# Kernel optimization log

Measured on AMD Instinct MI355X. Metric: run time of the kernel, lower is better.

## Reference

```python
import jax, jax.numpy as jnp
import numpy as np

N_NODES = 500000
N_EDGES = 16000000
IN_DIM = 17


def setup_inputs() -> dict:
    key = jax.random.key(0)
    k1, k2, k3, k4, k5, k6, k7 = jax.random.split(key, 7)
    x = jax.random.normal(k1, (N_NODES, IN_DIM), dtype=jnp.float32)
    edge_index = jax.random.randint(k2, (2, N_EDGES), 0, N_NODES, dtype=jnp.int64)
    edge_weight = jax.random.uniform(k3, (N_EDGES,), dtype=jnp.float32)
    # SAGEConv(17, 1): lin_l applied to aggregated neighbors (with bias),
    # lin_r applied to root features (no bias, PyG convention).
    s = 1.0 / np.sqrt(IN_DIM)
    w_l = jax.random.uniform(k4, (1, IN_DIM), minval=-s, maxval=s, dtype=jnp.float32)
    b_l = jax.random.uniform(k5, (1,), minval=-s, maxval=s, dtype=jnp.float32)
    w_r = jax.random.uniform(k6, (1, IN_DIM), minval=-s, maxval=s, dtype=jnp.float32)
    # out: Linear(1, 1)
    k8, k9 = jax.random.split(k7)
    w_o = jax.random.uniform(k8, (1, 1), minval=-1.0, maxval=1.0, dtype=jnp.float32)
    b_o = jax.random.uniform(k9, (1,), minval=-1.0, maxval=1.0, dtype=jnp.float32)
    return {"x": x, "edge_index": edge_index, "edge_weight": edge_weight,
            "w_l": w_l, "b_l": b_l, "w_r": w_r, "w_o": w_o, "b_o": b_o}


def reference(x, edge_index, edge_weight, w_l, b_l, w_r, w_o, b_o):
    # SAGEConv (mean aggregation). edge_weight is unused (faithful to PyG SAGEConv).
    # Project to out_dim=1 BEFORE aggregation (linearity makes this exact and
    # avoids materializing a [E,17] gathered buffer):
    #   lin_l(mean_j x_j) + b_l == mean_j (x_j @ W_l^T) + b_l
    src, dst = edge_index[0], edge_index[1]
    x_proj_l = x @ w_l.T                      # [N, 1]
    msg = x_proj_l[src, 0]                    # [E]  gathered source projections
    agg = jax.ops.segment_sum(msg, dst, num_segments=x.shape[0])          # [N]
    cnt = jax.ops.segment_sum(jnp.ones_like(msg), dst, num_segments=x.shape[0])
    mean = agg / jnp.maximum(cnt, 1.0)        # zero for isolated nodes
    h = mean[:, None] + b_l + x @ w_r.T       # [N, 1]  lin_l(aggr) + lin_r(x)
    h = jax.nn.elu(h)
    return h @ w_o.T + b_o                    # [N, 1]
```

## Files before the change

kernel.cpp:

```cpp
#include <hip/hip_runtime.h>
#include <hip/hip_bf16.h>
#include <math.h>

#define IN_DIM 17
#define NB 128
#define LOG_BN 12
#define BN 4096
#define K_SPLIT 16
#define CHUNK 8192
#define EPT 32
#define VAL_SCALE 4096.0f
#define FP_SCALE 268435456.0f
#define FP_INV   (1.0 / 268435456.0)

__global__ void node_proj_kernel(const float* __restrict__ x,
                                 const float* __restrict__ w_l,
                                 const float* __restrict__ w_r,
                                 float* __restrict__ p_l,
                                 float* __restrict__ p_r,
                                 int n_nodes) {
    int i = blockIdx.x * blockDim.x + threadIdx.x;
    if (i >= n_nodes) return;
    const float* row = x + (size_t)i * IN_DIM;
    float sl = 0.0f, sr = 0.0f;
#pragma unroll
    for (int k = 0; k < IN_DIM; ++k) {
        float v = row[k];
        sl = fmaf(v, w_l[k], sl);
        sr = fmaf(v, w_r[k], sr);
    }
    p_l[i] = sl;
    p_r[i] = sr;
}

__global__ __launch_bounds__(256, 4)
void sort_scatter_kernel(const int* __restrict__ src,
                         const int* __restrict__ dst,
                         const float* __restrict__ p_l,
                         unsigned* __restrict__ staging,
                         unsigned short* __restrict__ segtab,
                         int n_edges) {
    __shared__ unsigned cnt[NB];
    __shared__ unsigned sstart[NB + 1];
    __shared__ unsigned lbuf[CHUNK];

    const int tid = threadIdx.x;
    const int blk = blockIdx.x;
    const int e0 = blk * CHUNK;
    const int chunk_n = min(CHUNK, n_edges - e0);
    const int nvec = chunk_n >> 2;

    for (int t = tid; t < NB; t += 256) cnt[t] = 0;
    __syncthreads();

    uint4 dreg[EPT / 4];
    uint4 sreg[EPT / 4];
    unsigned rpack[EPT / 2];
    const uint4* dv = (const uint4*)(dst + e0);
    const uint4* sv = (const uint4*)(src + e0);
#pragma unroll
    for (int k = 0; k < EPT / 4; ++k) {
        int q = tid + k * 256;
        if (q < nvec) {
            uint4 d = dv[q];
            dreg[k] = d;
            sreg[k] = sv[q];
            unsigned r0 = atomicAdd(&cnt[d.x >> LOG_BN], 1u);
            unsigned r1 = atomicAdd(&cnt[d.y >> LOG_BN], 1u);
            unsigned r2 = atomicAdd(&cnt[d.z >> LOG_BN], 1u);
            unsigned r3 = atomicAdd(&cnt[d.w >> LOG_BN], 1u);
            rpack[2 * k]     = r0 | (r1 << 16);
            rpack[2 * k + 1] = r2 | (r3 << 16);
        }
    }
    unsigned tail_rank = 0;
    {
        int i = (nvec << 2) + tid;
        if (i < chunk_n)
            tail_rank = atomicAdd(&cnt[(unsigned)dst[e0 + i] >> LOG_BN], 1u);
    }
    __syncthreads();

    if (tid < 64) {
        unsigned c0 = cnt[tid], c1 = cnt[tid + 64];
        unsigned s0 = c0;
#pragma unroll
        for (int off = 1; off < 64; off <<= 1) {
            unsigned v = __shfl_up(s0, off);
            if (tid >= off) s0 += v;
        }
        unsigned tot0 = __shfl(s0, 63);
        unsigned s1 = c1;
#pragma unroll
        for (int off = 1; off < 64; off <<= 1) {
            unsigned v = __shfl_up(s1, off);
            if (tid >= off) s1 += v;
        }
        s1 += tot0;
        sstart[tid + 1] = s0;
        sstart[tid + 65] = s1;
        if (tid == 0) sstart[0] = 0;
    }
    __syncthreads();

    for (int t = tid; t <= NB; t += 256)
        segtab[(size_t)blk * (NB + 2) + t] = (unsigned short)sstart[t];

#pragma unroll
    for (int k = 0; k < EPT / 4; ++k) {
        int q = tid + k * 256;
        if (q < nvec) {
            uint4 s = sreg[k];
            uint4 d = dreg[k];
            float pf[4] = {p_l[s.x], p_l[s.y], p_l[s.z], p_l[s.w]};
            unsigned dd[4] = {d.x, d.y, d.z, d.w};
            unsigned rk[4] = {rpack[2 * k] & 0xFFFFu, rpack[2 * k] >> 16,
                              rpack[2 * k + 1] & 0xFFFFu, rpack[2 * k + 1] >> 16};
#pragma unroll
            for (int u = 0; u < 4; ++u) {
                int fx = __float2int_rn(pf[u] * VAL_SCALE);
                fx = max(-32768, min(32767, fx));
                unsigned entry = ((unsigned)(fx & 0xFFFF) << 16) | (dd[u] & (BN - 1));
                unsigned b = dd[u] >> LOG_BN;
                lbuf[sstart[b] + rk[u]] = entry;
            }
        }
    }
    {
        int i = (nvec << 2) + tid;
        if (i < chunk_n) {
            unsigned s = (unsigned)src[e0 + i];
            unsigned d = (unsigned)dst[e0 + i];
            int fx = __float2int_rn(p_l[s] * VAL_SCALE);
            fx = max(-32768, min(32767, fx));
            unsigned entry = ((unsigned)(fx & 0xFFFF) << 16) | (d & (BN - 1));
            lbuf[sstart[d >> LOG_BN] + tail_rank] = entry;
        }
    }
    __syncthreads();

    uint4* outp = (uint4*)(staging + (size_t)blk * CHUNK);
    const uint4* lp = (const uint4*)lbuf;
    int nv4 = (chunk_n + 3) >> 2;
    for (int q = tid; q < nv4; q += 256)
        outp[q] = lp[q];
}

__global__ __launch_bounds__(256, 4)
void reduce_kernel(const unsigned* __restrict__ staging,
                   const unsigned short* __restrict__ segtab,
                   unsigned* __restrict__ bins,
                   int nblk) {
    __shared__ unsigned lds_p[BN];
    const int tid = threadIdx.x;
    const int b = blockIdx.x / K_SPLIT;
    const int j = blockIdx.x % K_SPLIT;
    const int wave = tid >> 6, lane = tid & 63;

    for (int i = tid; i < BN; i += 256) lds_p[i] = 0u;
    __syncthreads();

    const int blk0 = (int)((long long)nblk * j / K_SPLIT);
    const int blk1 = (int)((long long)nblk * (j + 1) / K_SPLIT);

    int blk = blk0 + wave;
    unsigned sA = 0, eA = 0, sB = 0, eB = 0;
    unsigned enA0 = 0, enA1 = 0;
    if (blk < blk1) {
        const unsigned short* st = segtab + (size_t)blk * (NB + 2) + b;
        sA = st[0]; eA = st[1];
    }
    if (blk + 4 < blk1) {
        const unsigned short* st = segtab + (size_t)(blk + 4) * (NB + 2) + b;
        sB = st[0]; eB = st[1];
    }
    if (blk < blk1) {
        const unsigned* sp = staging + (size_t)blk * CHUNK;
        unsigned i0 = sA + lane;
        if (i0 < eA) enA0 = sp[i0];
        unsigned i1 = i0 + 64;
        if (i1 < eA) enA1 = sp[i1];
    }

    while (blk < blk1) {
        unsigned sC = 0, eC = 0;
        if (blk + 8 < blk1) {
            const unsigned short* st = segtab + (size_t)(blk + 8) * (NB + 2) + b;
            sC = st[0]; eC = st[1];
        }
        unsigned enB0 = 0, enB1 = 0;
        if (blk + 4 < blk1) {
            const unsigned* spn = staging + (size_t)(blk + 4) * CHUNK;
            unsigned i0 = sB + lane;
            if (i0 < eB) enB0 = spn[i0];
            unsigned i1 = i0 + 64;
            if (i1 < eB) enB1 = spn[i1];
        }
        {
            unsigned i0 = sA + lane;
            if (i0 < eA) {
                int v = (int)(short)(enA0 >> 16);
                atomicAdd(&lds_p[enA0 & (BN - 1)], ((unsigned)v << 8) | 1u);
            }
            unsigned i1 = i0 + 64;
            if (i1 < eA) {
                int v = (int)(short)(enA1 >> 16);
                atomicAdd(&lds_p[enA1 & (BN - 1)], ((unsigned)v << 8) | 1u);
            }
            if (sA + 128 < eA) {
                const unsigned* sp = staging + (size_t)blk * CHUNK;
                for (unsigned i = sA + 128 + lane; i < eA; i += 64) {
                    unsigned en = sp[i];
                    int v = (int)(short)(en >> 16);
                    atomicAdd(&lds_p[en & (BN - 1)], ((unsigned)v << 8) | 1u);
                }
            }
        }
        asm volatile("" :: "v"(enB0), "v"(enB1), "v"(sC), "v"(eC));
        blk += 4;
        sA = sB; eA = eB; enA0 = enB0; enA1 = enB1;
        sB = sC; eB = eC;
    }
    __syncthreads();
    unsigned* gb = bins + (size_t)b * BN;
    for (int i = tid; i < BN; i += 256) {
        unsigned v = lds_p[i];
        if (v) atomicAdd(&gb[i], v);
    }
}

__global__ void finalize_kernel(const float* __restrict__ p_r,
                                const unsigned* __restrict__ bins,
                                const float* __restrict__ b_l,
                                const float* __restrict__ w_o,
                                const float* __restrict__ b_o,
                                float* __restrict__ out,
                                int n_nodes) {
    int i = blockIdx.x * blockDim.x + threadIdx.x;
    if (i >= n_nodes) return;
    unsigned u = bins[i];
    int sum24 = ((int)u) >> 8;
    int cnt = (int)(u & 0xFFu);
    float sum = (float)sum24 * (1.0f / VAL_SCALE);
    float mean = sum / fmaxf((float)cnt, 1.0f);
    float h = mean + b_l[0] + p_r[i];
    h = (h > 0.0f) ? h : expm1f(h);
    out[i] = fmaf(h, w_o[0], b_o[0]);
}

__global__ void edge_scatter_fb(const int* __restrict__ edge_index,
                                const float* __restrict__ p_l,
                                unsigned long long* __restrict__ bins,
                                int n_edges) {
    int e = blockIdx.x * blockDim.x + threadIdx.x;
    if (e >= n_edges) return;
    int s = edge_index[e];
    int d = edge_index[n_edges + e];
    float p = p_l[s];
    long long sfx = (long long)llrintf(p * FP_SCALE);
    unsigned long long delta = ((unsigned long long)sfx << 20) | 1ULL;
    atomicAdd(&bins[d], delta);
}

__global__ void finalize_fb(const float* __restrict__ p_r,
                            const unsigned long long* __restrict__ bins,
                            const float* __restrict__ b_l,
                            const float* __restrict__ w_o,
                            const float* __restrict__ b_o,
                            float* __restrict__ out,
                            int n_nodes) {
    int i = blockIdx.x * blockDim.x + threadIdx.x;
    if (i >= n_nodes) return;
    long long packed = (long long)bins[i];
    int cntv = (int)(packed & 0xFFFFFLL);
    long long sfx = packed >> 20;
    float sum = (float)((double)sfx * FP_INV);
    float mean = sum / fmaxf((float)cntv, 1.0f);
    float h = mean + b_l[0] + p_r[i];
    h = (h > 0.0f) ? h : expm1f(h);
    out[i] = fmaf(h, w_o[0], b_o[0]);
}

static inline size_t align_up(size_t v, size_t a) { return (v + a - 1) & ~(a - 1); }

extern "C" void kernel_launch(void* const* d_in, const int* in_sizes, int n_in,
                              void* d_out, int out_size, void* d_ws, size_t ws_size,
                              hipStream_t stream) {
    const float* x   = (const float*)d_in[0];
    const int*   ei  = (const int*)d_in[1];
    const float* w_l = (const float*)d_in[3];
    const float* b_l = (const float*)d_in[4];
    const float* w_r = (const float*)d_in[5];
    const float* w_o = (const float*)d_in[6];
    const float* b_o = (const float*)d_in[7];
    float* out = (float*)d_out;

    const int n_nodes = in_sizes[0] / IN_DIM;
    const int n_edges = in_sizes[2];
    const int* src = ei;
    const int* dst = ei + n_edges;
    const int nblk = (n_edges + CHUNK - 1) / CHUNK;

    char* ws = (char*)d_ws;
    size_t off = 0;
    size_t o_pl = off;      off = align_up(off + (size_t)n_nodes * 4, 256);
    size_t o_pr = off;      off = align_up(off + (size_t)n_nodes * 4, 256);
    size_t o_stage = off;   off = align_up(off + (size_t)nblk * CHUNK * 4, 256);
    size_t o_seg = off;     off = align_up(off + (size_t)nblk * (NB + 2) * 2, 256);
    size_t o_bins = off;    off = align_up(off + (size_t)NB * BN * 4, 256);
    size_t need = off;

    float* p_l = (float*)(ws + o_pl);
    float* p_r = (float*)(ws + o_pr);

    const int B = 256;
    node_proj_kernel<<<(n_nodes + B - 1) / B, B, 0, stream>>>(x, w_l, w_r, p_l, p_r, n_nodes);

    if (ws_size >= need) {
        unsigned* staging       = (unsigned*)(ws + o_stage);
        unsigned short* segtab  = (unsigned short*)(ws + o_seg);
        unsigned* bins          = (unsigned*)(ws + o_bins);

        hipMemsetAsync(bins, 0, (size_t)NB * BN * 4, stream);
        sort_scatter_kernel<<<nblk, B, 0, stream>>>(src, dst, p_l, staging, segtab, n_edges);
        reduce_kernel<<<NB * K_SPLIT, B, 0, stream>>>(staging, segtab, bins, nblk);
        finalize_kernel<<<(n_nodes + B - 1) / B, B, 0, stream>>>(p_r, bins, b_l, w_o, b_o,
                                                                 out, n_nodes);
    } else {
        unsigned long long* bins_fb = (unsigned long long*)(ws + o_stage);
        hipMemsetAsync(bins_fb, 0, (size_t)n_nodes * 8, stream);
        edge_scatter_fb<<<(n_edges + B - 1) / B, B, 0, stream>>>(ei, p_l, bins_fb, n_edges);
        finalize_fb<<<(n_nodes + B - 1) / B, B, 0, stream>>>(p_r, bins_fb, b_l, w_o, b_o,
                                                             out, n_nodes);
    }
}
```

Measured before the change: 348.0 us.

## Assign 8-lane groups per staging chunk in reduce kernel, halve K_SPLIT

```diff
diff --git a/kernel.cpp b/kernel.cpp
--- a/kernel.cpp
+++ b/kernel.cpp
@@ -6,7 +6,8 @@
 #define NB 128
 #define LOG_BN 12
 #define BN 4096
-#define K_SPLIT 16
+#define K_SPLIT 8
+#define GRP 8
 #define CHUNK 8192
 #define EPT 32
 #define VAL_SCALE 4096.0f
@@ -155,71 +156,35 @@
     const int tid = threadIdx.x;
     const int b = blockIdx.x / K_SPLIT;
     const int j = blockIdx.x % K_SPLIT;
-    const int wave = tid >> 6, lane = tid & 63;
+    const int grp = tid >> 3;
+    const int sub = tid & (GRP - 1);
 
     for (int i = tid; i < BN; i += 256) lds_p[i] = 0u;
     __syncthreads();
 
-    const int blk0 = (int)((long long)nblk * j / K_SPLIT);
-    const int blk1 = (int)((long long)nblk * (j + 1) / K_SPLIT);
-
-    int blk = blk0 + wave;
-    unsigned sA = 0, eA = 0, sB = 0, eB = 0;
-    unsigned enA0 = 0, enA1 = 0;
-    if (blk < blk1) {
-        const unsigned short* st = segtab + (size_t)blk * (NB + 2) + b;
-        sA = st[0]; eA = st[1];
-    }
-    if (blk + 4 < blk1) {
-        const unsigned short* st = segtab + (size_t)(blk + 4) * (NB + 2) + b;
-        sB = st[0]; eB = st[1];
-    }
-    if (blk < blk1) {
-        const unsigned* sp = staging + (size_t)blk * CHUNK;
-        unsigned i0 = sA + lane;
-        if (i0 < eA) enA0 = sp[i0];
-        unsigned i1 = i0 + 64;
-        if (i1 < eA) enA1 = sp[i1];
-    }
-
-    while (blk < blk1) {
-        unsigned sC = 0, eC = 0;
-        if (blk + 8 < blk1) {
-            const unsigned short* st = segtab + (size_t)(blk + 8) * (NB + 2) + b;
-            sC = st[0]; eC = st[1];
-        }
-        unsigned enB0 = 0, enB1 = 0;
-        if (blk + 4 < blk1) {
-            const unsigned* spn = staging + (size_t)(blk + 4) * CHUNK;
-            unsigned i0 = sB + lane;
-            if (i0 < eB) enB0 = spn[i0];
-            unsigned i1 = i0 + 64;
-            if (i1 < eB) enB1 = spn[i1];
-        }
-        {
-            unsigned i0 = sA + lane;
-            if (i0 < eA) {
-                int v = (int)(short)(enA0 >> 16);
-                atomicAdd(&lds_p[enA0 & (BN - 1)], ((unsigned)v << 8) | 1u);
-            }
-            unsigned i1 = i0 + 64;
-            if (i1 < eA) {
-                int v = (int)(short)(enA1 >> 16);
-                atomicAdd(&lds_p[enA1 & (BN - 1)], ((unsigned)v << 8) | 1u);
-            }
-            if (sA + 128 < eA) {
-                const unsigned* sp = staging + (size_t)blk * CHUNK;
-                for (unsigned i = sA + 128 + lane; i < eA; i += 64) {
-                    unsigned en = sp[i];
-                    int v = (int)(short)(en >> 16);
-                    atomicAdd(&lds_p[en & (BN - 1)], ((unsigned)v << 8) | 1u);
-                }
-            }
-        }
-        asm volatile("" :: "v"(enB0), "v"(enB1), "v"(sC), "v"(eC));
-        blk += 4;
-        sA = sB; eA = eB; enA0 = enB0; enA1 = enB1;
-        sB = sC; eB = eC;
+    const int c0 = (int)((long long)nblk * j / K_SPLIT);
+    const int c1 = (int)((long long)nblk * (j + 1) / K_SPLIT);
+
+    int c = c0 + grp;
+    unsigned s_nxt = 0, e_nxt = 0;
+    if (c < c1) {
+        const unsigned short* st = segtab + (size_t)c * (NB + 2) + b;
+        s_nxt = st[0]; e_nxt = st[1];
+    }
+    while (c < c1) {
+        unsigned s = s_nxt, e = e_nxt;
+        const int cn = c + 32;
+        if (cn < c1) {
+            const unsigned short* st = segtab + (size_t)cn * (NB + 2) + b;
+            s_nxt = st[0]; e_nxt = st[1];
+        }
+        const unsigned* sp = staging + (size_t)c * CHUNK;
+        for (unsigned i = s + sub; i < e; i += GRP) {
+            unsigned en = sp[i];
+            int v = (int)(short)(en >> 16);
+            atomicAdd(&lds_p[en & (BN - 1)], ((unsigned)v << 8) | 1u);
+        }
+        c = cn;
     }
     __syncthreads();
     unsigned* gb = bins + (size_t)b * BN;
```

New measurement: 343.2 us. Within noise of the previous version (-1.4%).
